# Optimization experiments

Hardware: AMD Instinct MI355X
Metric: run time of the kernel (lower is better)

## Reference

```python
import jax, jax.numpy as jnp
import numpy as np


def setup_inputs() -> dict:
    key = jax.random.key(0)
    ks = jax.random.split(key, 6)
    B, C, H, W = 4, 64, 96, 96
    IC = C // 2
    return {
        "x": jax.random.normal(ks[0], (B, C, H, W), dtype=jnp.float32),
        "y": jax.random.normal(ks[1], (B, C, H, W), dtype=jnp.float32),
        "w_phi": jax.random.normal(ks[2], (IC, C), dtype=jnp.float32) * 0.05,
        "w_theta": jax.random.normal(ks[3], (IC, C), dtype=jnp.float32) * 0.05,
        "w_g": jax.random.normal(ks[4], (IC, C), dtype=jnp.float32) * 0.05,
        "w_mask": jax.random.normal(ks[5], (C, IC), dtype=jnp.float32) * 0.05,
    }


def reference(x, y, w_phi, w_theta, w_g, w_mask):
    # x, y: [B, C, H, W]; 1x1 convs (no bias) are channel GEMMs.
    B, C, H, W = x.shape
    IC = C // 2
    # conv outputs have IC channels, but the original views them as (B, C, -1),
    # i.e. token axis N = IC*H*W / C = H*W/2, feature axis C. Replicate exactly.
    phi = jnp.einsum('bchw,oc->bohw', x, w_phi).reshape(B, C, -1)          # [B, C, N]
    theta = jnp.einsum('bchw,oc->bohw', y, w_theta).reshape(B, C, -1)      # [B, C, N]
    theta = jnp.transpose(theta, (0, 2, 1))                                # [B, N, C]
    g = jnp.einsum('bchw,oc->bohw', x, w_g).reshape(B, C, -1)              # [B, C, N]
    g = jnp.transpose(g, (0, 2, 1))                                        # [B, N, C]
    scores = jnp.einsum('bnc,bcm->bnm', theta, phi)                        # [B, N, N]
    attn = jax.nn.softmax(scores, axis=1)  # softmax over dim=1 (rows), per original
    out = jnp.einsum('bnm,bmc->bnc', attn, g)                              # [B, N, C]
    out = jnp.transpose(out, (0, 2, 1)).reshape(B, IC, H, W)               # [B, IC, H, W]
    mask = jnp.einsum('bchw,oc->bohw', out, w_mask)                        # [B, C, H, W]
    return mask + x
```

## Files before the change

### kernel.cpp

```cpp
#include <hip/hip_runtime.h>

#define NTOK 4608
#define CCH  64
#define HWSZ 9216
#define NB   4
#define NSPL 8
#define NCHT (NTOK/32)
#define L2E  1.4426950408889634f

typedef unsigned short u16;
typedef __attribute__((ext_vector_type(4))) short s16x4;
typedef __attribute__((ext_vector_type(8))) short s16x8;
typedef __attribute__((ext_vector_type(4))) float f32x4;

__device__ __forceinline__ f32x4 mfma16(s16x8 a, s16x8 b, f32x4 c){
  return __builtin_amdgcn_mfma_f32_16x16x32_bf16(a, b, c, 0, 0, 0);
}
__device__ __forceinline__ short f2bfh(float f){
  __bf16 h = (__bf16)f;
  return (short)__builtin_bit_cast(unsigned short, h);
}
__device__ __forceinline__ float bf2f(u16 h){
  return __uint_as_float(((unsigned int)h) << 16);
}
__device__ __forceinline__ float ex2(float x){
  return __builtin_amdgcn_exp2f(x);
}

__device__ __forceinline__ void gload16(const void* g, void* l){
  __builtin_amdgcn_global_load_lds(
      (const __attribute__((address_space(1))) void*)g,
      (__attribute__((address_space(3))) void*)l, 16, 0, 0);
}
#define SBAR() __builtin_amdgcn_sched_barrier(0)
#define WAITVM(N) do{ SBAR(); asm volatile("s_waitcnt vmcnt(" #N ")" ::: "memory"); SBAR(); }while(0)
#define PRIO(N) __builtin_amdgcn_s_setprio(N)

__global__ __launch_bounds__(512) void proj_kernel(
    const float* __restrict__ x, const float* __restrict__ y,
    const float* __restrict__ w_phi, const float* __restrict__ w_theta,
    const float* __restrict__ w_g,
    u16* __restrict__ TH, u16* __restrict__ PH, u16* __restrict__ G){
  const int b = blockIdx.y;
  const int n = blockIdx.x*64 + (threadIdx.x & 63);
  const int wq = __builtin_amdgcn_readfirstlane((int)(threadIdx.x >> 6));
  const float* xb = x + (size_t)b*CCH*HWSZ;
  const float* yb = y + (size_t)b*CCH*HWSZ;
  const float* wp = w_phi   + wq*4*CCH;
  const float* wt = w_theta + wq*4*CCH;
  const float* wg = w_g     + wq*4*CCH;
  float accP[8], accT[8], accG[8];
  #pragma unroll
  for(int j=0;j<8;++j){ accP[j]=0.f; accT[j]=0.f; accG[j]=0.f; }
  for(int k=0;k<CCH;k+=4){
    float xv0[4], xv1[4], yv0[4], yv1[4];
    #pragma unroll
    for(int u=0;u<4;++u){
      xv0[u] = xb[(size_t)(k+u)*HWSZ + n];
      xv1[u] = xb[(size_t)(k+u)*HWSZ + NTOK + n];
      yv0[u] = yb[(size_t)(k+u)*HWSZ + n];
      yv1[u] = yb[(size_t)(k+u)*HWSZ + NTOK + n];
    }
    #pragma unroll
    for(int u=0;u<4;++u)
      #pragma unroll
      for(int j=0;j<8;++j){
        float xv = (j&1)?xv1[u]:xv0[u];
        accP[j] = fmaf(wp[(j>>1)*CCH + k+u], xv, accP[j]);
        accT[j] = fmaf(wt[(j>>1)*CCH + k+u], (j&1)?yv1[u]:yv0[u], accT[j]);
        accG[j] = fmaf(wg[(j>>1)*CCH + k+u], xv, accG[j]);
      }
  }
  s16x8 vp, vt;
  #pragma unroll
  for(int j=0;j<8;++j){
    vp[j]=f2bfh(accP[j]);
    vt[j]=f2bfh(accT[j]*L2E);
  }
  *(s16x8*)(PH + ((size_t)b*NTOK + n)*CCH + wq*8) = vp;
  *(s16x8*)(TH + ((size_t)b*NTOK + n)*CCH + wq*8) = vt;
  #pragma unroll
  for(int j=0;j<8;++j)
    G[((size_t)b*CCH + wq*8 + j)*NTOK + n] = f2bfh(accG[j]);
}

__global__ __launch_bounds__(256, 4) void passA_kernel(
    const u16* __restrict__ TH, const u16* __restrict__ PH,
    float* __restrict__ CSUMP){
  __shared__ __align__(16) u16 ldsTH[4*4096];
  const int bid = blockIdx.x;
  const int xcd = bid & 7, b = xcd >> 1;
  const int j = ((bid >> 3) << 1) | (xcd & 1);
  const int part = j & (NSPL-1);
  const int mt = j >> 3;
  const int lane = threadIdx.x & 63;
  const int wq = __builtin_amdgcn_readfirstlane((int)(threadIdx.x >> 6));
  const int l15 = lane & 15, lg = lane >> 4;
  const int mbase = mt*128 + wq*32;
  const u16* thb = TH + (size_t)b*NTOK*CCH;
  const u16* phb = PH + (size_t)b*NTOK*CCH;
  const u16* p0 = phb + (size_t)(mbase + l15)*CCH + lg*8;
  const u16* p1 = p0 + 16*CCH;
  s16x8 bf00 = *(const s16x8*)p0, bf01 = *(const s16x8*)(p0+32);
  s16x8 bf10 = *(const s16x8*)p1, bf11 = *(const s16x8*)(p1+32);
  float rs0 = 0.f, rs1 = 0.f;

  const int NCH = (NTOK/NSPL)/64;
  const int n0 = part*(NTOK/NSPL);
  const int srl0 = wq*16 + (lane>>3);
  const int ssl0 = (lane&7) ^ (srl0&7);
  const int srl1 = srl0 + 8;
  const int ssl1 = (lane&7) ^ (srl1&7);
  auto STAGE = [&](int ci, int bi){
    const u16* base = thb + (size_t)(n0 + ci*64)*CCH;
    gload16(base + (size_t)srl0*CCH + ssl0*8, ldsTH + bi*4096 + wq*1024);
    gload16(base + (size_t)srl1*CCH + ssl1*8, ldsTH + bi*4096 + wq*1024 + 512);
  };

  STAGE(0, 0); SBAR();
  STAGE(1, 1); SBAR();
  #pragma unroll 1
  for(int t=0; t<NCH; ++t){
    int ci = t+2; if(ci >= NCH) ci -= NCH;
    STAGE(ci, (t+2)&3);
    WAITVM(4);
    __builtin_amdgcn_s_barrier();
    const u16* bTH = ldsTH + (t&3)*4096;
    #pragma unroll
    for(int s=0;s<4;++s){
      const int r = s*16 + l15, rx = r & 7;
      const u16* rb = bTH + r*64;
      s16x8 a0 = *(const s16x8*)(rb + ((lg     ^ rx)<<3));
      s16x8 a1 = *(const s16x8*)(rb + (((lg+4) ^ rx)<<3));
      f32x4 v0 = {0.f,0.f,0.f,0.f}, v1 = {0.f,0.f,0.f,0.f};
      PRIO(1);
      v0 = mfma16(a0, bf00, v0); v0 = mfma16(a1, bf01, v0);
      v1 = mfma16(a0, bf10, v1); v1 = mfma16(a1, bf11, v1);
      PRIO(0);
      rs0 += (ex2(v0[0])+ex2(v0[1])) + (ex2(v0[2])+ex2(v0[3]));
      rs1 += (ex2(v1[0])+ex2(v1[1])) + (ex2(v1[2])+ex2(v1[3]));
    }
  }

  rs0 += __shfl_xor(rs0, 16); rs0 += __shfl_xor(rs0, 32);
  rs1 += __shfl_xor(rs1, 16); rs1 += __shfl_xor(rs1, 32);
  if(lg == 0){
    float* dst = CSUMP + (size_t)(part*NB + b)*NTOK + mbase;
    dst[l15]      = rs0;
    dst[16 + l15] = rs1;
  }
}

__global__ __launch_bounds__(256) void scale_g_kernel(
    const u16* __restrict__ G, const float* __restrict__ CSUMP,
    u16* __restrict__ G2){
  __shared__ float dinv[32];
  const int tid = threadIdx.x;
  const int ch = blockIdx.x % NCHT;
  const int b  = blockIdx.x / NCHT;
  const int m0 = ch*32;
  if(tid < 32){
    float s = 0.f;
    #pragma unroll
    for(int h=0;h<NSPL;++h) s += CSUMP[(size_t)(h*NB+b)*NTOK + m0 + tid];
    dinv[tid] = 1.0f/s;
  }
  __syncthreads();
  const int c  = tid & 63;
  const int lg = tid >> 6;
  const u16* gr = G + ((size_t)b*CCH + c)*NTOK + m0;
  s16x4 lo = *(const s16x4*)(gr + 4*lg);
  s16x4 hi = *(const s16x4*)(gr + 16 + 4*lg);
  s16x8 o;
  #pragma unroll
  for(int k=0;k<4;++k){
    o[k]   = f2bfh(bf2f((u16)lo[k]) * dinv[4*lg+k]);
    o[4+k] = f2bfh(bf2f((u16)hi[k]) * dinv[16+4*lg+k]);
  }
  *(s16x8*)(G2 + ((((size_t)b*NCHT + ch)*4 + lg)*CCH + c)*8) = o;
}

template<int MSPLIT>
__global__ __launch_bounds__(256, 4) void passB_kernel(
    const u16* __restrict__ TH, const u16* __restrict__ PH,
    const u16* __restrict__ G2, u16* __restrict__ OUTPB){
  __shared__ __align__(16) u16 ldsPH[4*2048];
  const int bid = blockIdx.x;
  const int xcd = bid & 7, b = xcd >> 1;
  const int j = ((bid >> 3) << 1) | (xcd & 1);
  const int mpart = j % MSPLIT;
  const int nt = j / MSPLIT;
  const int lane = threadIdx.x & 63;
  const int wq = __builtin_amdgcn_readfirstlane((int)(threadIdx.x >> 6));
  const int l15 = lane & 15, lg = lane >> 4;
  const int nbase = nt*128 + wq*32;
  const u16* thb = TH + (size_t)b*NTOK*CCH;
  const u16* phb = PH + (size_t)b*NTOK*CCH;
  const u16* g2b = G2 + (size_t)b*NCHT*4*CCH*8;
  const u16* t0 = thb + (size_t)(nbase + l15)*CCH + lg*8;
  const u16* t1 = t0 + 16*CCH;
  s16x8 bt00 = *(const s16x8*)t0, bt01 = *(const s16x8*)(t0+32);
  s16x8 bt10 = *(const s16x8*)t1, bt11 = *(const s16x8*)(t1+32);
  f32x4 acc[2][4];
  #pragma unroll
  for(int n2=0;n2<2;++n2)
    #pragma unroll
    for(int ct=0;ct<4;++ct) acc[n2][ct] = (f32x4){0.f,0.f,0.f,0.f};

  const int mcnt = NTOK/MSPLIT;
  const int NCH = mcnt/32;
  const int ch0 = (mpart*mcnt)/32;

  const int srl = wq*8 + (lane>>3);
  const int ssl = (lane&7) ^ (srl&7);
  auto STAGE_PH = [&](int ci, int bi){
    gload16(phb + (size_t)((ch0+ci)*32 + srl)*CCH + ssl*8,
            ldsPH + bi*2048 + wq*512);
  };

  STAGE_PH(0, 0); SBAR();
  STAGE_PH(1, 1); SBAR();
  #pragma unroll 1
  for(int t=0; t<NCH; ++t){
    WAITVM(1);
    __builtin_amdgcn_s_barrier();
    const u16* gp = g2b + ((size_t)((ch0+t)*4 + lg)*CCH + l15)*8;
    s16x8 g0 = *(const s16x8*)(gp);
    s16x8 g1 = *(const s16x8*)(gp + 128);
    s16x8 g2 = *(const s16x8*)(gp + 256);
    s16x8 g3 = *(const s16x8*)(gp + 384);
    SBAR();
    int c2 = t+2; if(c2 >= NCH) c2 -= NCH;
    STAGE_PH(c2, (t+2)&3);
    SBAR();
    const u16* bPH = ldsPH + (t&3)*2048;
    const int rx = l15 & 7;
    const u16* rb0 = bPH + l15*64;
    const u16* rb1 = rb0 + 16*64;
    s16x8 ap00 = *(const s16x8*)(rb0 + ((lg     ^ rx)<<3));
    s16x8 ap01 = *(const s16x8*)(rb0 + (((lg+4) ^ rx)<<3));
    s16x8 ap10 = *(const s16x8*)(rb1 + ((lg     ^ rx)<<3));
    s16x8 ap11 = *(const s16x8*)(rb1 + (((lg+4) ^ rx)<<3));
    f32x4 s00={0.f,0.f,0.f,0.f}, s01={0.f,0.f,0.f,0.f};
    f32x4 s10={0.f,0.f,0.f,0.f}, s11={0.f,0.f,0.f,0.f};
    PRIO(1);
    s00 = mfma16(ap00, bt00, s00); s00 = mfma16(ap01, bt01, s00);
    s01 = mfma16(ap10, bt00, s01); s01 = mfma16(ap11, bt01, s01);
    s10 = mfma16(ap00, bt10, s10); s10 = mfma16(ap01, bt11, s10);
    s11 = mfma16(ap10, bt10, s11); s11 = mfma16(ap11, bt11, s11);
    PRIO(0);
    s16x8 pa0, pa1;
    #pragma unroll
    for(int r=0;r<4;++r){
      pa0[r]   = f2bfh(ex2(s00[r]));
      pa0[4+r] = f2bfh(ex2(s01[r]));
      pa1[r]   = f2bfh(ex2(s10[r]));
      pa1[4+r] = f2bfh(ex2(s11[r]));
    }
    PRIO(1);
    acc[0][0] = mfma16(pa0, g0, acc[0][0]);
    acc[1][0] = mfma16(pa1, g0, acc[1][0]);
    acc[0][1] = mfma16(pa0, g1, acc[0][1]);
    acc[1][1] = mfma16(pa1, g1, acc[1][1]);
    acc[0][2] = mfma16(pa0, g2, acc[0][2]);
    acc[1][2] = mfma16(pa1, g2, acc[1][2]);
    acc[0][3] = mfma16(pa0, g3, acc[0][3]);
    acc[1][3] = mfma16(pa1, g3, acc[1][3]);
    PRIO(0);
  }

  u16* outp = OUTPB + ((size_t)(mpart*NB + b)*NTOK)*CCH;
  #pragma unroll
  for(int n2=0;n2<2;++n2)
    #pragma unroll
    for(int ct=0;ct<4;++ct)
      #pragma unroll
      for(int r=0;r<4;++r)
        outp[(size_t)(nbase + n2*16 + lg*4 + r)*CCH + ct*16 + l15] =
            (u16)f2bfh(acc[n2][ct][r]);
}

__global__ __launch_bounds__(256) void reduce_kernel(
    const u16* __restrict__ OUTPB, u16* __restrict__ OUTS, int msplit){
  const int gid = blockIdx.x*256 + threadIdx.x;
  const size_t stride8 = (size_t)NB*NTOK*CCH/8;
  const s16x8* src = (const s16x8*)OUTPB;
  float a[8];
  s16x8 u0 = src[gid];
  #pragma unroll
  for(int k=0;k<8;++k) a[k] = bf2f((u16)u0[k]);
  for(int h=1; h<msplit; ++h){
    s16x8 u = src[(size_t)h*stride8 + gid];
    #pragma unroll
    for(int k=0;k<8;++k) a[k] += bf2f((u16)u[k]);
  }
  s16x8 o;
  #pragma unroll
  for(int k=0;k<8;++k) o[k] = f2bfh(a[k]);
  ((s16x8*)OUTS)[gid] = o;
}

__global__ __launch_bounds__(512, 2) void conv_kernel(
    const u16* __restrict__ OUTS, const float* __restrict__ w_mask,
    const float* __restrict__ x, float* __restrict__ out){
  const int b = blockIdx.y;
  const int nl = threadIdx.x & 63;
  const int n = blockIdx.x*64 + nl;
  const int q = __builtin_amdgcn_readfirstlane((int)(threadIdx.x >> 6));
  const s16x8* vr = (const s16x8*)(OUTS + ((size_t)b*NTOK + n)*CCH);
  float v[64];
  #pragma unroll
  for(int k=0;k<8;++k){
    s16x8 u = vr[k];
    #pragma unroll
    for(int e=0;e<8;++e) v[k*8+e] = bf2f((u16)u[e]);
  }
  const float* wm = w_mask + q*8*32;
  #pragma unroll
  for(int jj=0;jj<8;++jj){
    float a0 = 0.f, a1 = 0.f;
    #pragma unroll
    for(int ic=0;ic<32;++ic){
      float w = wm[jj*32 + ic];
      a0 = fmaf(w, v[2*ic],   a0);
      a1 = fmaf(w, v[2*ic+1], a1);
    }
    const size_t idx = ((size_t)b*CCH + q*8 + jj)*HWSZ + n;
    out[idx]        = a0 + x[idx];
    out[idx + NTOK] = a1 + x[idx + NTOK];
  }
}

extern "C" void kernel_launch(void* const* d_in, const int* in_sizes, int n_in,
                              void* d_out, int out_size, void* d_ws, size_t ws_size,
                              hipStream_t stream){
  const float* x       = (const float*)d_in[0];
  const float* y       = (const float*)d_in[1];
  const float* w_phi   = (const float*)d_in[2];
  const float* w_theta = (const float*)d_in[3];
  const float* w_g     = (const float*)d_in[4];
  const float* w_mask  = (const float*)d_in[5];
  float* out = (float*)d_out;
  char* ws = (char*)d_ws;

  const size_t projB  = (size_t)NB*NTOK*CCH*sizeof(u16);
  const size_t fstat  = (size_t)NB*NTOK*sizeof(float);
  const size_t fixed  = 5*projB + (size_t)NSPL*fstat;

  int msplit = (ws_size >= fixed + 8*projB) ? 8
             : (ws_size >= fixed + 4*projB) ? 4 : 2;

  size_t off = 0;
  u16*   TH    = (u16*)(ws + off); off += projB;
  u16*   PH    = (u16*)(ws + off); off += projB;
  u16*   G     = (u16*)(ws + off); off += projB;
  u16*   G2    = (u16*)(ws + off); off += projB;
  u16*   OUTPB = (u16*)(ws + off); off += (size_t)msplit*projB;
  u16*   OUTS  = (u16*)(ws + off); off += projB;
  float* CSUMP = (float*)(ws + off); off += (size_t)NSPL*fstat;

  proj_kernel<<<dim3(NTOK/64, NB), 512, 0, stream>>>(x, y, w_phi, w_theta, w_g,
                                                     TH, PH, G);
  passA_kernel<<<dim3((NTOK/128)*NSPL*NB), 256, 0, stream>>>(TH, PH, CSUMP);
  scale_g_kernel<<<dim3(NB*NCHT), 256, 0, stream>>>(G, CSUMP, G2);
  const int gB = (NTOK/128)*msplit*NB;
  switch(msplit){
    case 8: passB_kernel<8><<<dim3(gB),256,0,stream>>>(TH,PH,G2,OUTPB); break;
    case 4: passB_kernel<4><<<dim3(gB),256,0,stream>>>(TH,PH,G2,OUTPB); break;
    default: passB_kernel<2><<<dim3(gB),256,0,stream>>>(TH,PH,G2,OUTPB); break;
  }
  reduce_kernel<<<dim3((NB*NTOK*CCH/8)/256), 256, 0, stream>>>(OUTPB, OUTS, msplit);
  conv_kernel<<<dim3(NTOK/64, NB), 512, 0, stream>>>(OUTS, w_mask, x, out);
}
```

Baseline: 98.53 us.

## Fuse split-K reduction into mask conv and widen passA column tiles

Result: slower. 116.2 us (+18.0%).

```diff
diff --git a/kernel.cpp b/kernel.cpp
--- a/kernel.cpp
+++ b/kernel.cpp
@@ -4,7 +4,7 @@
 #define CCH  64
 #define HWSZ 9216
 #define NB   4
-#define NSPL 8
+#define NSPL 12
 #define NCHT (NTOK/32)
 #define L2E  1.4426950408889634f
 
@@ -91,19 +91,22 @@
   const int bid = blockIdx.x;
   const int xcd = bid & 7, b = xcd >> 1;
   const int j = ((bid >> 3) << 1) | (xcd & 1);
-  const int part = j & (NSPL-1);
-  const int mt = j >> 3;
+  const int part = j % NSPL;
+  const int mt = j / NSPL;
   const int lane = threadIdx.x & 63;
   const int wq = __builtin_amdgcn_readfirstlane((int)(threadIdx.x >> 6));
   const int l15 = lane & 15, lg = lane >> 4;
-  const int mbase = mt*128 + wq*32;
+  const int mbase = mt*256 + wq*64;
   const u16* thb = TH + (size_t)b*NTOK*CCH;
   const u16* phb = PH + (size_t)b*NTOK*CCH;
-  const u16* p0 = phb + (size_t)(mbase + l15)*CCH + lg*8;
-  const u16* p1 = p0 + 16*CCH;
-  s16x8 bf00 = *(const s16x8*)p0, bf01 = *(const s16x8*)(p0+32);
-  s16x8 bf10 = *(const s16x8*)p1, bf11 = *(const s16x8*)(p1+32);
-  float rs0 = 0.f, rs1 = 0.f;
+  s16x8 bfr[4][2];
+  #pragma unroll
+  for(int t2=0;t2<4;++t2){
+    const u16* p = phb + (size_t)(mbase + t2*16 + l15)*CCH + lg*8;
+    bfr[t2][0] = *(const s16x8*)p;
+    bfr[t2][1] = *(const s16x8*)(p+32);
+  }
+  float rs0=0.f, rs1=0.f, rs2=0.f, rs3=0.f;
 
   const int NCH = (NTOK/NSPL)/64;
   const int n0 = part*(NTOK/NSPL);
@@ -132,22 +135,31 @@
       const u16* rb = bTH + r*64;
       s16x8 a0 = *(const s16x8*)(rb + ((lg     ^ rx)<<3));
       s16x8 a1 = *(const s16x8*)(rb + (((lg+4) ^ rx)<<3));
-      f32x4 v0 = {0.f,0.f,0.f,0.f}, v1 = {0.f,0.f,0.f,0.f};
+      f32x4 v0={0.f,0.f,0.f,0.f}, v1={0.f,0.f,0.f,0.f};
+      f32x4 v2={0.f,0.f,0.f,0.f}, v3={0.f,0.f,0.f,0.f};
       PRIO(1);
-      v0 = mfma16(a0, bf00, v0); v0 = mfma16(a1, bf01, v0);
-      v1 = mfma16(a0, bf10, v1); v1 = mfma16(a1, bf11, v1);
+      v0 = mfma16(a0, bfr[0][0], v0); v0 = mfma16(a1, bfr[0][1], v0);
+      v1 = mfma16(a0, bfr[1][0], v1); v1 = mfma16(a1, bfr[1][1], v1);
+      v2 = mfma16(a0, bfr[2][0], v2); v2 = mfma16(a1, bfr[2][1], v2);
+      v3 = mfma16(a0, bfr[3][0], v3); v3 = mfma16(a1, bfr[3][1], v3);
       PRIO(0);
       rs0 += (ex2(v0[0])+ex2(v0[1])) + (ex2(v0[2])+ex2(v0[3]));
       rs1 += (ex2(v1[0])+ex2(v1[1])) + (ex2(v1[2])+ex2(v1[3]));
+      rs2 += (ex2(v2[0])+ex2(v2[1])) + (ex2(v2[2])+ex2(v2[3]));
+      rs3 += (ex2(v3[0])+ex2(v3[1])) + (ex2(v3[2])+ex2(v3[3]));
     }
   }
 
   rs0 += __shfl_xor(rs0, 16); rs0 += __shfl_xor(rs0, 32);
   rs1 += __shfl_xor(rs1, 16); rs1 += __shfl_xor(rs1, 32);
+  rs2 += __shfl_xor(rs2, 16); rs2 += __shfl_xor(rs2, 32);
+  rs3 += __shfl_xor(rs3, 16); rs3 += __shfl_xor(rs3, 32);
   if(lg == 0){
     float* dst = CSUMP + (size_t)(part*NB + b)*NTOK + mbase;
     dst[l15]      = rs0;
     dst[16 + l15] = rs1;
+    dst[32 + l15] = rs2;
+    dst[48 + l15] = rs3;
   }
 }
 
@@ -280,40 +292,27 @@
             (u16)f2bfh(acc[n2][ct][r]);
 }
 
-__global__ __launch_bounds__(256) void reduce_kernel(
-    const u16* __restrict__ OUTPB, u16* __restrict__ OUTS, int msplit){
-  const int gid = blockIdx.x*256 + threadIdx.x;
-  const size_t stride8 = (size_t)NB*NTOK*CCH/8;
-  const s16x8* src = (const s16x8*)OUTPB;
-  float a[8];
-  s16x8 u0 = src[gid];
-  #pragma unroll
-  for(int k=0;k<8;++k) a[k] = bf2f((u16)u0[k]);
-  for(int h=1; h<msplit; ++h){
-    s16x8 u = src[(size_t)h*stride8 + gid];
-    #pragma unroll
-    for(int k=0;k<8;++k) a[k] += bf2f((u16)u[k]);
-  }
-  s16x8 o;
-  #pragma unroll
-  for(int k=0;k<8;++k) o[k] = f2bfh(a[k]);
-  ((s16x8*)OUTS)[gid] = o;
-}
-
+template<int MSPLIT>
 __global__ __launch_bounds__(512, 2) void conv_kernel(
-    const u16* __restrict__ OUTS, const float* __restrict__ w_mask,
+    const u16* __restrict__ OUTPB, const float* __restrict__ w_mask,
     const float* __restrict__ x, float* __restrict__ out){
   const int b = blockIdx.y;
   const int nl = threadIdx.x & 63;
   const int n = blockIdx.x*64 + nl;
   const int q = __builtin_amdgcn_readfirstlane((int)(threadIdx.x >> 6));
-  const s16x8* vr = (const s16x8*)(OUTS + ((size_t)b*NTOK + n)*CCH);
   float v[64];
   #pragma unroll
-  for(int k=0;k<8;++k){
-    s16x8 u = vr[k];
-    #pragma unroll
-    for(int e=0;e<8;++e) v[k*8+e] = bf2f((u16)u[e]);
+  for(int c=0;c<64;++c) v[c] = 0.f;
+  #pragma unroll
+  for(int h=0; h<MSPLIT; ++h){
+    const s16x8* vr = (const s16x8*)(OUTPB + ((size_t)(h*NB + b)*NTOK + n)*CCH);
+    s16x8 u[8];
+    #pragma unroll
+    for(int k=0;k<8;++k) u[k] = vr[k];
+    #pragma unroll
+    for(int k=0;k<8;++k)
+      #pragma unroll
+      for(int e=0;e<8;++e) v[k*8+e] += bf2f((u16)u[k][e]);
   }
   const float* wm = w_mask + q*8*32;
   #pragma unroll
@@ -345,7 +344,7 @@
 
   const size_t projB  = (size_t)NB*NTOK*CCH*sizeof(u16);
   const size_t fstat  = (size_t)NB*NTOK*sizeof(float);
-  const size_t fixed  = 5*projB + (size_t)NSPL*fstat;
+  const size_t fixed  = 4*projB + (size_t)NSPL*fstat;
 
   int msplit = (ws_size >= fixed + 8*projB) ? 8
              : (ws_size >= fixed + 4*projB) ? 4 : 2;
@@ -356,12 +355,11 @@
   u16*   G     = (u16*)(ws + off); off += projB;
   u16*   G2    = (u16*)(ws + off); off += projB;
   u16*   OUTPB = (u16*)(ws + off); off += (size_t)msplit*projB;
-  u16*   OUTS  = (u16*)(ws + off); off += projB;
   float* CSUMP = (float*)(ws + off); off += (size_t)NSPL*fstat;
 
   proj_kernel<<<dim3(NTOK/64, NB), 512, 0, stream>>>(x, y, w_phi, w_theta, w_g,
                                                      TH, PH, G);
-  passA_kernel<<<dim3((NTOK/128)*NSPL*NB), 256, 0, stream>>>(TH, PH, CSUMP);
+  passA_kernel<<<dim3((NTOK/256)*NSPL*NB), 256, 0, stream>>>(TH, PH, CSUMP);
   scale_g_kernel<<<dim3(NB*NCHT), 256, 0, stream>>>(G, CSUMP, G2);
   const int gB = (NTOK/128)*msplit*NB;
   switch(msplit){
@@ -369,6 +367,9 @@
     case 4: passB_kernel<4><<<dim3(gB),256,0,stream>>>(TH,PH,G2,OUTPB); break;
     default: passB_kernel<2><<<dim3(gB),256,0,stream>>>(TH,PH,G2,OUTPB); break;
   }
-  reduce_kernel<<<dim3((NB*NTOK*CCH/8)/256), 256, 0, stream>>>(OUTPB, OUTS, msplit);
-  conv_kernel<<<dim3(NTOK/64, NB), 512, 0, stream>>>(OUTS, w_mask, x, out);
-}
+  switch(msplit){
+    case 8: conv_kernel<8><<<dim3(NTOK/64,NB),512,0,stream>>>(OUTPB,w_mask,x,out); break;
+    case 4: conv_kernel<4><<<dim3(NTOK/64,NB),512,0,stream>>>(OUTPB,w_mask,x,out); break;
+    default: conv_kernel<2><<<dim3(NTOK/64,NB),512,0,stream>>>(OUTPB,w_mask,x,out); break;
+  }
+}
```

## Give each wave private LDS staging buffers to drop block barriers in attention passes

Applied to the files above, without the earlier changes.

New measurement: 104.3 us. +5.9%, slower.

```diff
diff --git a/kernel.cpp b/kernel.cpp
--- a/kernel.cpp
+++ b/kernel.cpp
@@ -84,10 +84,10 @@
     G[((size_t)b*CCH + wq*8 + j)*NTOK + n] = f2bfh(accG[j]);
 }
 
-__global__ __launch_bounds__(256, 4) void passA_kernel(
+__global__ __launch_bounds__(256, 3) void passA_kernel(
     const u16* __restrict__ TH, const u16* __restrict__ PH,
     float* __restrict__ CSUMP){
-  __shared__ __align__(16) u16 ldsTH[4*4096];
+  __shared__ __align__(16) u16 ldsTH[4][3*2048];
   const int bid = blockIdx.x;
   const int xcd = bid & 7, b = xcd >> 1;
   const int j = ((bid >> 3) << 1) | (xcd & 1);
@@ -105,16 +105,18 @@
   s16x8 bf10 = *(const s16x8*)p1, bf11 = *(const s16x8*)(p1+32);
   float rs0 = 0.f, rs1 = 0.f;
 
-  const int NCH = (NTOK/NSPL)/64;
+  const int NCH = (NTOK/NSPL)/32;
   const int n0 = part*(NTOK/NSPL);
-  const int srl0 = wq*16 + (lane>>3);
-  const int ssl0 = (lane&7) ^ (srl0&7);
-  const int srl1 = srl0 + 8;
-  const int ssl1 = (lane&7) ^ (srl1&7);
+  const int rl = lane >> 3;
+  const int sl = (lane & 7) ^ rl;
+  u16* wbuf = ldsTH[wq];
   auto STAGE = [&](int ci, int bi){
-    const u16* base = thb + (size_t)(n0 + ci*64)*CCH;
-    gload16(base + (size_t)srl0*CCH + ssl0*8, ldsTH + bi*4096 + wq*1024);
-    gload16(base + (size_t)srl1*CCH + ssl1*8, ldsTH + bi*4096 + wq*1024 + 512);
+    const u16* base = thb + (size_t)(n0 + ci*32 + rl)*CCH + sl*8;
+    u16* dst = wbuf + bi*2048;
+    gload16(base,            dst);
+    gload16(base +  8*CCH,   dst + 512);
+    gload16(base + 16*CCH,   dst + 1024);
+    gload16(base + 24*CCH,   dst + 1536);
   };
 
   STAGE(0, 0); SBAR();
@@ -122,12 +124,11 @@
   #pragma unroll 1
   for(int t=0; t<NCH; ++t){
     int ci = t+2; if(ci >= NCH) ci -= NCH;
-    STAGE(ci, (t+2)&3);
-    WAITVM(4);
-    __builtin_amdgcn_s_barrier();
-    const u16* bTH = ldsTH + (t&3)*4096;
-    #pragma unroll
-    for(int s=0;s<4;++s){
+    STAGE(ci, (t+2)%3);
+    WAITVM(8);
+    const u16* bTH = wbuf + (t%3)*2048;
+    #pragma unroll
+    for(int s=0;s<2;++s){
       const int r = s*16 + l15, rx = r & 7;
       const u16* rb = bTH + r*64;
       s16x8 a0 = *(const s16x8*)(rb + ((lg     ^ rx)<<3));
@@ -181,10 +182,10 @@
 }
 
 template<int MSPLIT>
-__global__ __launch_bounds__(256, 4) void passB_kernel(
+__global__ __launch_bounds__(256, 3) void passB_kernel(
     const u16* __restrict__ TH, const u16* __restrict__ PH,
     const u16* __restrict__ G2, u16* __restrict__ OUTPB){
-  __shared__ __align__(16) u16 ldsPH[4*2048];
+  __shared__ __align__(16) u16 ldsPH[4][3*2048];
   const int bid = blockIdx.x;
   const int xcd = bid & 7, b = xcd >> 1;
   const int j = ((bid >> 3) << 1) | (xcd & 1);
@@ -211,19 +212,22 @@
   const int NCH = mcnt/32;
   const int ch0 = (mpart*mcnt)/32;
 
-  const int srl = wq*8 + (lane>>3);
-  const int ssl = (lane&7) ^ (srl&7);
+  const int rl = lane >> 3;
+  const int sl = (lane & 7) ^ rl;
+  u16* wbuf = ldsPH[wq];
   auto STAGE_PH = [&](int ci, int bi){
-    gload16(phb + (size_t)((ch0+ci)*32 + srl)*CCH + ssl*8,
-            ldsPH + bi*2048 + wq*512);
+    const u16* base = phb + (size_t)((ch0+ci)*32 + rl)*CCH + sl*8;
+    u16* dst = wbuf + bi*2048;
+    gload16(base,            dst);
+    gload16(base +  8*CCH,   dst + 512);
+    gload16(base + 16*CCH,   dst + 1024);
+    gload16(base + 24*CCH,   dst + 1536);
   };
 
   STAGE_PH(0, 0); SBAR();
   STAGE_PH(1, 1); SBAR();
   #pragma unroll 1
   for(int t=0; t<NCH; ++t){
-    WAITVM(1);
-    __builtin_amdgcn_s_barrier();
     const u16* gp = g2b + ((size_t)((ch0+t)*4 + lg)*CCH + l15)*8;
     s16x8 g0 = *(const s16x8*)(gp);
     s16x8 g1 = *(const s16x8*)(gp + 128);
@@ -231,9 +235,9 @@
     s16x8 g3 = *(const s16x8*)(gp + 384);
     SBAR();
     int c2 = t+2; if(c2 >= NCH) c2 -= NCH;
-    STAGE_PH(c2, (t+2)&3);
-    SBAR();
-    const u16* bPH = ldsPH + (t&3)*2048;
+    STAGE_PH(c2, (t+2)%3);
+    WAITVM(12);
+    const u16* bPH = wbuf + (t%3)*2048;
     const int rx = l15 & 7;
     const u16* rb0 = bPH + l15*64;
     const u16* rb1 = rb0 + 16*64;
@@ -347,8 +351,7 @@
   const size_t fstat  = (size_t)NB*NTOK*sizeof(float);
   const size_t fixed  = 5*projB + (size_t)NSPL*fstat;
 
-  int msplit = (ws_size >= fixed + 8*projB) ? 8
-             : (ws_size >= fixed + 4*projB) ? 4 : 2;
+  int msplit = (ws_size >= fixed + 8*projB) ? 8 : 4;
 
   size_t off = 0;
   u16*   TH    = (u16*)(ws + off); off += projB;
@@ -365,9 +368,8 @@
   scale_g_kernel<<<dim3(NB*NCHT), 256, 0, stream>>>(G, CSUMP, G2);
   const int gB = (NTOK/128)*msplit*NB;
   switch(msplit){
-    case 8: passB_kernel<8><<<dim3(gB),256,0,stream>>>(TH,PH,G2,OUTPB); break;
-    case 4: passB_kernel<4><<<dim3(gB),256,0,stream>>>(TH,PH,G2,OUTPB); break;
-    default: passB_kernel<2><<<dim3(gB),256,0,stream>>>(TH,PH,G2,OUTPB); break;
+    case 8:  passB_kernel<8><<<dim3(gB),256,0,stream>>>(TH,PH,G2,OUTPB); break;
+    default: passB_kernel<4><<<dim3(gB),256,0,stream>>>(TH,PH,G2,OUTPB); break;
   }
   reduce_kernel<<<dim3((NB*NTOK*CCH/8)/256), 256, 0, stream>>>(OUTPB, OUTS, msplit);
   conv_kernel<<<dim3(NTOK/64, NB), 512, 0, stream>>>(OUTS, w_mask, x, out);
```

## Replace split-K partial buffers and reduce kernel with fp32 atomic accumulation

Applied to the files above, without the earlier changes.

Result: slower. 115.1 us (+16.9%).

```diff
diff --git a/kernel.cpp b/kernel.cpp
--- a/kernel.cpp
+++ b/kernel.cpp
@@ -6,6 +6,7 @@
 #define NB   4
 #define NSPL 8
 #define NCHT (NTOK/32)
+#define MSPL 8
 #define L2E  1.4426950408889634f
 
 typedef unsigned short u16;
@@ -40,10 +41,17 @@
     const float* __restrict__ x, const float* __restrict__ y,
     const float* __restrict__ w_phi, const float* __restrict__ w_theta,
     const float* __restrict__ w_g,
-    u16* __restrict__ TH, u16* __restrict__ PH, u16* __restrict__ G){
+    u16* __restrict__ TH, u16* __restrict__ PH, u16* __restrict__ G,
+    float* __restrict__ OUTS){
   const int b = blockIdx.y;
   const int n = blockIdx.x*64 + (threadIdx.x & 63);
   const int wq = __builtin_amdgcn_readfirstlane((int)(threadIdx.x >> 6));
+  {
+    f32x4* zp = (f32x4*)(OUTS + ((size_t)b*NTOK + (size_t)blockIdx.x*64)*CCH);
+    f32x4 z = {0.f,0.f,0.f,0.f};
+    zp[threadIdx.x*2]   = z;
+    zp[threadIdx.x*2+1] = z;
+  }
   const float* xb = x + (size_t)b*CCH*HWSZ;
   const float* yb = y + (size_t)b*CCH*HWSZ;
   const float* wp = w_phi   + wq*4*CCH;
@@ -180,16 +188,15 @@
   *(s16x8*)(G2 + ((((size_t)b*NCHT + ch)*4 + lg)*CCH + c)*8) = o;
 }
 
-template<int MSPLIT>
 __global__ __launch_bounds__(256, 4) void passB_kernel(
     const u16* __restrict__ TH, const u16* __restrict__ PH,
-    const u16* __restrict__ G2, u16* __restrict__ OUTPB){
+    const u16* __restrict__ G2, float* __restrict__ OUTS){
   __shared__ __align__(16) u16 ldsPH[4*2048];
   const int bid = blockIdx.x;
   const int xcd = bid & 7, b = xcd >> 1;
   const int j = ((bid >> 3) << 1) | (xcd & 1);
-  const int mpart = j % MSPLIT;
-  const int nt = j / MSPLIT;
+  const int mpart = j % MSPL;
+  const int nt = j / MSPL;
   const int lane = threadIdx.x & 63;
   const int wq = __builtin_amdgcn_readfirstlane((int)(threadIdx.x >> 6));
   const int l15 = lane & 15, lg = lane >> 4;
@@ -207,7 +214,7 @@
     #pragma unroll
     for(int ct=0;ct<4;++ct) acc[n2][ct] = (f32x4){0.f,0.f,0.f,0.f};
 
-  const int mcnt = NTOK/MSPLIT;
+  const int mcnt = NTOK/MSPL;
   const int NCH = mcnt/32;
   const int ch0 = (mpart*mcnt)/32;
 
@@ -269,51 +276,30 @@
     PRIO(0);
   }
 
-  u16* outp = OUTPB + ((size_t)(mpart*NB + b)*NTOK)*CCH;
+  float* outp = OUTS + ((size_t)b*NTOK)*CCH;
   #pragma unroll
   for(int n2=0;n2<2;++n2)
     #pragma unroll
     for(int ct=0;ct<4;++ct)
       #pragma unroll
       for(int r=0;r<4;++r)
-        outp[(size_t)(nbase + n2*16 + lg*4 + r)*CCH + ct*16 + l15] =
-            (u16)f2bfh(acc[n2][ct][r]);
-}
-
-__global__ __launch_bounds__(256) void reduce_kernel(
-    const u16* __restrict__ OUTPB, u16* __restrict__ OUTS, int msplit){
-  const int gid = blockIdx.x*256 + threadIdx.x;
-  const size_t stride8 = (size_t)NB*NTOK*CCH/8;
-  const s16x8* src = (const s16x8*)OUTPB;
-  float a[8];
-  s16x8 u0 = src[gid];
-  #pragma unroll
-  for(int k=0;k<8;++k) a[k] = bf2f((u16)u0[k]);
-  for(int h=1; h<msplit; ++h){
-    s16x8 u = src[(size_t)h*stride8 + gid];
-    #pragma unroll
-    for(int k=0;k<8;++k) a[k] += bf2f((u16)u[k]);
-  }
-  s16x8 o;
-  #pragma unroll
-  for(int k=0;k<8;++k) o[k] = f2bfh(a[k]);
-  ((s16x8*)OUTS)[gid] = o;
+        atomicAdd(&outp[(size_t)(nbase + n2*16 + lg*4 + r)*CCH + ct*16 + l15],
+                  acc[n2][ct][r]);
 }
 
 __global__ __launch_bounds__(512, 2) void conv_kernel(
-    const u16* __restrict__ OUTS, const float* __restrict__ w_mask,
+    const float* __restrict__ OUTS, const float* __restrict__ w_mask,
     const float* __restrict__ x, float* __restrict__ out){
   const int b = blockIdx.y;
   const int nl = threadIdx.x & 63;
   const int n = blockIdx.x*64 + nl;
   const int q = __builtin_amdgcn_readfirstlane((int)(threadIdx.x >> 6));
-  const s16x8* vr = (const s16x8*)(OUTS + ((size_t)b*NTOK + n)*CCH);
+  const f32x4* vr = (const f32x4*)(OUTS + ((size_t)b*NTOK + n)*CCH);
   float v[64];
   #pragma unroll
-  for(int k=0;k<8;++k){
-    s16x8 u = vr[k];
-    #pragma unroll
-    for(int e=0;e<8;++e) v[k*8+e] = bf2f((u16)u[e]);
+  for(int k=0;k<16;++k){
+    f32x4 u = vr[k];
+    v[4*k]=u[0]; v[4*k+1]=u[1]; v[4*k+2]=u[2]; v[4*k+3]=u[3];
   }
   const float* wm = w_mask + q*8*32;
   #pragma unroll
@@ -344,31 +330,21 @@
   char* ws = (char*)d_ws;
 
   const size_t projB  = (size_t)NB*NTOK*CCH*sizeof(u16);
+  const size_t outsB  = (size_t)NB*NTOK*CCH*sizeof(float);
   const size_t fstat  = (size_t)NB*NTOK*sizeof(float);
-  const size_t fixed  = 5*projB + (size_t)NSPL*fstat;
-
-  int msplit = (ws_size >= fixed + 8*projB) ? 8
-             : (ws_size >= fixed + 4*projB) ? 4 : 2;
 
   size_t off = 0;
   u16*   TH    = (u16*)(ws + off); off += projB;
   u16*   PH    = (u16*)(ws + off); off += projB;
   u16*   G     = (u16*)(ws + off); off += projB;
   u16*   G2    = (u16*)(ws + off); off += projB;
-  u16*   OUTPB = (u16*)(ws + off); off += (size_t)msplit*projB;
-  u16*   OUTS  = (u16*)(ws + off); off += projB;
+  float* OUTS  = (float*)(ws + off); off += outsB;
   float* CSUMP = (float*)(ws + off); off += (size_t)NSPL*fstat;
 
   proj_kernel<<<dim3(NTOK/64, NB), 512, 0, stream>>>(x, y, w_phi, w_theta, w_g,
-                                                     TH, PH, G);
+                                                     TH, PH, G, OUTS);
   passA_kernel<<<dim3((NTOK/128)*NSPL*NB), 256, 0, stream>>>(TH, PH, CSUMP);
   scale_g_kernel<<<dim3(NB*NCHT), 256, 0, stream>>>(G, CSUMP, G2);
-  const int gB = (NTOK/128)*msplit*NB;
-  switch(msplit){
-    case 8: passB_kernel<8><<<dim3(gB),256,0,stream>>>(TH,PH,G2,OUTPB); break;
-    case 4: passB_kernel<4><<<dim3(gB),256,0,stream>>>(TH,PH,G2,OUTPB); break;
-    default: passB_kernel<2><<<dim3(gB),256,0,stream>>>(TH,PH,G2,OUTPB); break;
-  }
-  reduce_kernel<<<dim3((NB*NTOK*CCH/8)/256), 256, 0, stream>>>(OUTPB, OUTS, msplit);
+  passB_kernel<<<dim3((NTOK/128)*MSPL*NB), 256, 0, stream>>>(TH, PH, G2, OUTS);
   conv_kernel<<<dim3(NTOK/64, NB), 512, 0, stream>>>(OUTS, w_mask, x, out);
 }
```
